# Kernel tuning notes

Hardware: AMD Instinct MI355X
Metric: run time of the kernel (lower is better)

The kernel has to match this reference:

```python
import jax, jax.numpy as jnp
import numpy as np

N = 33554432  # 2**25 activations, 128 MB fp32
K = 1024      # winners kept


def setup_inputs() -> dict:
    key = jax.random.key(0)
    inputs = jax.random.normal(key, (N,), dtype=jnp.float32)
    return {"inputs": inputs, "k": K}


def reference(inputs, k):
    # k-th largest value = threshold (original: tf.sort desc, take element k-1)
    topk_vals, _ = jax.lax.top_k(inputs, k)
    threshold = topk_vals[k - 1]
    # zero out everything strictly below the threshold
    return jnp.where(inputs < threshold, jnp.zeros_like(inputs), inputs)
```

## Files before the change

kernel.cpp:

```cpp
#include <hip/hip_runtime.h>
#include <stdint.h>


#define HIST_BINS 4096
#define CTRL_OFF  HIST_BINS
#define CAND_OFF  (HIST_BINS + 16)

__device__ __forceinline__ uint32_t f2key(float x) {
  uint32_t u = __float_as_uint(x);
  return (u & 0x80000000u) ? ~u : (u | 0x80000000u);
}
__device__ __forceinline__ float key2f(uint32_t k) {
  uint32_t u = (k & 0x80000000u) ? (k & 0x7fffffffu) : ~k;
  return __uint_as_float(u);
}

__global__ void k_hist(const float4* __restrict__ in, int n4, int ntail,
                       const float* __restrict__ in_s,
                       uint32_t* __restrict__ ghist) {
  __shared__ uint32_t lh[HIST_BINS];
  for (int i = threadIdx.x; i < HIST_BINS; i += blockDim.x) lh[i] = 0;
  __syncthreads();
  int stride = gridDim.x * blockDim.x;
  for (int i = blockIdx.x * blockDim.x + threadIdx.x; i < n4; i += stride) {
    float4 v = in[i];
    atomicAdd(&lh[f2key(v.x) >> 20], 1u);
    atomicAdd(&lh[f2key(v.y) >> 20], 1u);
    atomicAdd(&lh[f2key(v.z) >> 20], 1u);
    atomicAdd(&lh[f2key(v.w) >> 20], 1u);
  }
  if (blockIdx.x == 0 && (int)threadIdx.x < ntail)
    atomicAdd(&lh[f2key(in_s[n4 * 4 + threadIdx.x]) >> 20], 1u);
  __syncthreads();
  for (int i = threadIdx.x; i < HIST_BINS; i += blockDim.x) {
    uint32_t c = lh[i];
    if (c) atomicAdd(&ghist[i], c);
  }
}

__global__ void k_select_bucket(const uint32_t* __restrict__ gh,
                                const int* __restrict__ kptr,
                                uint32_t* __restrict__ ctrl) {
  __shared__ uint32_t chunk[256];
  const int CPT = HIST_BINS / 256;
  int t = threadIdx.x;
  uint32_t s = 0;
  for (int i = 0; i < CPT; i++) s += gh[t * CPT + i];
  chunk[t] = s;
  __syncthreads();
  if (t == 0) {
    uint32_t K = (uint32_t)kptr[0];
    uint32_t above = 0;
    int sel = 0;
    for (int c = 255; c >= 0; c--) {
      if (above + chunk[c] >= K) { sel = c; break; }
      above += chunk[c];
    }
    int bsel = sel * CPT;
    for (int b = sel * CPT + CPT - 1; b >= sel * CPT; b--) {
      uint32_t c = gh[b];
      if (above + c >= K) { bsel = b; break; }
      above += c;
    }
    ctrl[1] = (uint32_t)bsel;
    ctrl[2] = K - above;
  }
}

__global__ void k_apply_gather(const float4* __restrict__ in,
                               float4* __restrict__ out, int n4, int ntail,
                               const float* __restrict__ in_s,
                               float* __restrict__ out_s,
                               uint32_t* __restrict__ ctrl,
                               uint32_t* __restrict__ keys,
                               uint32_t* __restrict__ idxs, uint32_t cap) {
  uint32_t sel = ctrl[1];
  int stride = gridDim.x * blockDim.x;
  for (int i = blockIdx.x * blockDim.x + threadIdx.x; i < n4; i += stride) {
    float4 v = in[i];
    uint32_t k0 = f2key(v.x), k1 = f2key(v.y), k2 = f2key(v.z), k3 = f2key(v.w);
    uint32_t b0 = k0 >> 20, b1 = k1 >> 20, b2 = k2 >> 20, b3 = k3 >> 20;
    float4 r;
    r.x = (b0 > sel) ? v.x : 0.0f;
    r.y = (b1 > sel) ? v.y : 0.0f;
    r.z = (b2 > sel) ? v.z : 0.0f;
    r.w = (b3 > sel) ? v.w : 0.0f;
    if (b0 == sel) { uint32_t p = atomicAdd(&ctrl[0], 1u); if (p < cap) { keys[p] = k0; idxs[p] = 4u * i + 0u; } }
    if (b1 == sel) { uint32_t p = atomicAdd(&ctrl[0], 1u); if (p < cap) { keys[p] = k1; idxs[p] = 4u * i + 1u; } }
    if (b2 == sel) { uint32_t p = atomicAdd(&ctrl[0], 1u); if (p < cap) { keys[p] = k2; idxs[p] = 4u * i + 2u; } }
    if (b3 == sel) { uint32_t p = atomicAdd(&ctrl[0], 1u); if (p < cap) { keys[p] = k3; idxs[p] = 4u * i + 3u; } }
    __builtin_nontemporal_store(r.x, &((float*)&out[i])[0]);
    __builtin_nontemporal_store(r.y, &((float*)&out[i])[1]);
    __builtin_nontemporal_store(r.z, &((float*)&out[i])[2]);
    __builtin_nontemporal_store(r.w, &((float*)&out[i])[3]);
  }
  if (blockIdx.x == 0 && (int)threadIdx.x < ntail) {
    int j = n4 * 4 + threadIdx.x;
    float x = in_s[j];
    uint32_t kk = f2key(x);
    uint32_t bb = kk >> 20;
    out_s[j] = (bb > sel) ? x : 0.0f;
    if (bb == sel) { uint32_t p = atomicAdd(&ctrl[0], 1u); if (p < cap) { keys[p] = kk; idxs[p] = (uint32_t)j; } }
  }
}

__global__ void __launch_bounds__(1024) k_final(uint32_t* __restrict__ ctrl,
                                                const uint32_t* __restrict__ keys,
                                                const uint32_t* __restrict__ idxs,
                                                uint32_t cap,
                                                float* __restrict__ out_s) {
  __shared__ uint32_t sh[8192];
  __shared__ uint32_t red[16];
  __shared__ uint32_t s_p, s_want;
  int t = threadIdx.x;
  uint32_t n = ctrl[0]; if (n > cap) n = cap;
  bool useLds = (n <= 8192);
  if (useLds) for (uint32_t i = t; i < n; i += blockDim.x) sh[i] = keys[i];
  if (t == 0) { s_p = ctrl[1] << 20; s_want = ctrl[2]; }
  __syncthreads();
  uint32_t p = s_p, want = s_want;
  for (int bit = 19; bit >= 0; bit--) {
    uint32_t test = p | (1u << bit);
    uint32_t hi = test >> bit;
    uint32_t cnt = 0;
    for (uint32_t i = t; i < n; i += blockDim.x) {
      uint32_t kk = useLds ? sh[i] : keys[i];
      cnt += ((kk >> bit) == hi) ? 1u : 0u;
    }
    for (int off = 32; off; off >>= 1) cnt += __shfl_down((int)cnt, off);
    int wave = t >> 6, lane = t & 63;
    if (lane == 0) red[wave] = cnt;
    __syncthreads();
    if (t == 0) {
      uint32_t tot = 0;
      for (int w = 0; w < 16; w++) tot += red[w];
      if (tot >= want) p = test; else want -= tot;
      s_p = p; s_want = want;
    }
    __syncthreads();
    p = s_p; want = s_want;
  }
  if (t == 0) ctrl[3] = __float_as_uint(key2f(p));
  for (uint32_t i = t; i < n; i += blockDim.x) {
    uint32_t kk = useLds ? sh[i] : keys[i];
    if (kk >= p) out_s[idxs[i]] = key2f(kk);
  }
}

extern "C" void kernel_launch(void* const* d_in, const int* in_sizes, int n_in,
                              void* d_out, int out_size, void* d_ws, size_t ws_size,
                              hipStream_t stream) {
  const float* in = (const float*)d_in[0];
  const int* kptr = (const int*)d_in[1];
  float* out = (float*)d_out;
  int n = in_sizes[0];
  int n4 = n >> 2;
  int ntail = n & 3;

  uint32_t* ws = (uint32_t*)d_ws;
  uint32_t* ghist = ws;
  uint32_t* ctrl = ws + CTRL_OFF;
  size_t ws_words = ws_size / 4;
  uint32_t cap = 0;
  if (ws_words > CAND_OFF + 2) cap = (uint32_t)((ws_words - CAND_OFF) / 2);
  uint32_t* keys = ws + CAND_OFF;
  uint32_t* idxs = keys + cap;

  hipMemsetAsync(d_ws, 0, CAND_OFF * sizeof(uint32_t), stream);

  k_hist<<<1024, 256, 0, stream>>>((const float4*)in, n4, ntail, in, ghist);
  k_select_bucket<<<1, 256, 0, stream>>>(ghist, kptr, ctrl);
  k_apply_gather<<<4096, 256, 0, stream>>>((const float4*)in, (float4*)out,
                                           n4, ntail, in, out, ctrl, keys, idxs, cap);
  k_final<<<1, 1024, 0, stream>>>(ctrl, keys, idxs, cap, out);
}
```

Before: 274.1 us.

## Sample input to bound histogram range, fuse bucket selection via last-block pattern

Adds a sampling kernel that builds a coarse 8-bit histogram from a subset of the input and picks a conservative lower cut bucket. The full 12-bit histogram pass then skips LDS atomics for elements below the cut, removing most of the contention from histogram updates. Bucket selection is folded into the last finishing block of the histogram kernel, which removes a separate launch. A fallback kernel redoes the full histogram if the sample-based cut was too high. The fallback adds an extra launch that exits early, plus a larger memset of the workspace.

```diff
diff --git a/kernel.cpp b/kernel.cpp
--- a/kernel.cpp
+++ b/kernel.cpp
@@ -3,8 +3,21 @@
 
 
 #define HIST_BINS 4096
-#define CTRL_OFF  HIST_BINS
-#define CAND_OFF  (HIST_BINS + 16)
+#define SAMPLE_BLOCKS 64
+#define SAMPLE_F4_PER_BLOCK 1024
+#define SAMPLE_M (SAMPLE_BLOCKS * SAMPLE_F4_PER_BLOCK * 4)
+
+#define TAIL_HIST_OFF 0
+#define FB_HIST_OFF   4096
+#define SAMP_HIST_OFF 8192
+#define DONE_SAMP     8448
+#define DONE_TAIL     8449
+#define DONE_FB       8450
+#define FB_FLAG       8451
+#define B8_OFF        8452
+#define CTRL_OFF      8456
+#define CAND_OFF      8472
+#define ZERO_WORDS    8472
 
 __device__ __forceinline__ uint32_t f2key(float x) {
   uint32_t u = __float_as_uint(x);
@@ -15,55 +28,181 @@
   return __uint_as_float(u);
 }
 
-__global__ void k_hist(const float4* __restrict__ in, int n4, int ntail,
-                       const float* __restrict__ in_s,
-                       uint32_t* __restrict__ ghist) {
+__device__ __forceinline__ void histAdd8(uint32_t* lh, uint32_t bin) {
+  unsigned long long peers = __ballot(1);
+#pragma unroll
+  for (int b = 0; b < 8; b++) {
+    unsigned long long vote = __ballot((bin >> b) & 1u);
+    peers &= ((bin >> b) & 1u) ? vote : ~vote;
+  }
+  unsigned lane = threadIdx.x & 63u;
+  if (lane == (unsigned)(__ffsll((long long)peers) - 1))
+    atomicAdd(&lh[bin], (uint32_t)__popcll(peers));
+}
+
+__device__ void select4096(const uint32_t* __restrict__ gh, uint32_t K,
+                           uint32_t* __restrict__ ctrl,
+                           uint32_t* __restrict__ fbflag,
+                           uint32_t* lh, uint32_t* chunk) {
+  int t = threadIdx.x;
+  for (int i = t; i < HIST_BINS; i += 256) lh[i] = gh[i];
+  __syncthreads();
+  uint32_t s = 0;
+#pragma unroll
+  for (int i = 0; i < 16; i++) s += lh[t * 16 + i];
+  chunk[t] = s;
+  __syncthreads();
+  if (t == 0) {
+    uint32_t above = 0;
+    int sel = -1;
+    for (int c = 255; c >= 0; c--) {
+      if (above + chunk[c] >= K) { sel = c; break; }
+      above += chunk[c];
+    }
+    if (sel < 0) {
+      if (fbflag) { *fbflag = 1u; }
+      else { ctrl[1] = 0u; ctrl[2] = 0xFFFFFFFFu; }
+    } else {
+      int bsel = sel * 16;
+      for (int b = sel * 16 + 15; b >= sel * 16; b--) {
+        uint32_t c = lh[b];
+        if (above + c >= K) { bsel = b; break; }
+        above += c;
+      }
+      ctrl[1] = (uint32_t)bsel;
+      ctrl[2] = K - above;
+    }
+  }
+}
+
+__global__ void k_sample(const float4* __restrict__ in, int n4,
+                         const int* __restrict__ kptr, uint32_t n,
+                         uint32_t* __restrict__ ws) {
+  __shared__ uint32_t lh[256];
+  __shared__ uint32_t s_last;
+  int t = threadIdx.x;
+  if (t < 256) lh[t] = 0;
+  __syncthreads();
+  if (n4 >= SAMPLE_F4_PER_BLOCK) {
+    int chunkf4 = n4 / SAMPLE_BLOCKS;
+    int base = blockIdx.x * chunkf4;
+    if (base + SAMPLE_F4_PER_BLOCK > n4) base = n4 - SAMPLE_F4_PER_BLOCK;
+#pragma unroll
+    for (int j = 0; j < 4; j++) {
+      float4 v = in[base + t + j * 256];
+      histAdd8(lh, f2key(v.x) >> 24);
+      histAdd8(lh, f2key(v.y) >> 24);
+      histAdd8(lh, f2key(v.z) >> 24);
+      histAdd8(lh, f2key(v.w) >> 24);
+    }
+  }
+  __syncthreads();
+  if (t < 256) {
+    uint32_t c = lh[t];
+    if (c) atomicAdd(&ws[SAMP_HIST_OFF + t], c);
+  }
+  __threadfence();
+  if (t == 0) s_last = atomicAdd(&ws[DONE_SAMP], 1u);
+  __syncthreads();
+  if (s_last == SAMPLE_BLOCKS - 1) {
+    __threadfence();
+    if (t < 256) lh[t] = ws[SAMP_HIST_OFF + t];
+    __syncthreads();
+    if (t == 0) {
+      int kv = kptr[0];
+      uint32_t K = (kv < 1) ? 1u : (uint32_t)kv;
+      uint64_t tgt64 = ((uint64_t)K * SAMPLE_M / (n ? n : 1u)) * 2u + 4096u;
+      uint32_t target = (tgt64 > SAMPLE_M) ? (uint32_t)SAMPLE_M : (uint32_t)tgt64;
+      if (target < 4096u) target = 4096u;
+      uint32_t sum = 0; uint32_t b8 = 0;
+      for (int b = 255; b >= 0; b--) {
+        sum += lh[b];
+        if (sum >= target) { b8 = (uint32_t)b; break; }
+      }
+      ws[B8_OFF] = b8;
+    }
+  }
+}
+
+__global__ void k_hist_tail(const float4* __restrict__ in, int n4, int ntail,
+                            const float* __restrict__ in_s,
+                            const int* __restrict__ kptr,
+                            uint32_t* __restrict__ ws, int nblocks, uint32_t n) {
   __shared__ uint32_t lh[HIST_BINS];
-  for (int i = threadIdx.x; i < HIST_BINS; i += blockDim.x) lh[i] = 0;
-  __syncthreads();
+  __shared__ uint32_t chunk[256];
+  __shared__ uint32_t s_last;
+  int t = threadIdx.x;
+  for (int i = t; i < HIST_BINS; i += blockDim.x) lh[i] = 0;
+  __syncthreads();
+  uint32_t cut = ws[B8_OFF] << 4;
   int stride = gridDim.x * blockDim.x;
-  for (int i = blockIdx.x * blockDim.x + threadIdx.x; i < n4; i += stride) {
+  for (int i = blockIdx.x * blockDim.x + t; i < n4; i += stride) {
+    float4 v = in[i];
+    uint32_t k0 = f2key(v.x) >> 20, k1 = f2key(v.y) >> 20;
+    uint32_t k2 = f2key(v.z) >> 20, k3 = f2key(v.w) >> 20;
+    if (k0 >= cut) atomicAdd(&lh[k0], 1u);
+    if (k1 >= cut) atomicAdd(&lh[k1], 1u);
+    if (k2 >= cut) atomicAdd(&lh[k2], 1u);
+    if (k3 >= cut) atomicAdd(&lh[k3], 1u);
+  }
+  if (blockIdx.x == 0 && t < ntail) {
+    uint32_t kk = f2key(in_s[n4 * 4 + t]) >> 20;
+    if (kk >= cut) atomicAdd(&lh[kk], 1u);
+  }
+  __syncthreads();
+  for (int i = t; i < HIST_BINS; i += blockDim.x) {
+    uint32_t c = lh[i];
+    if (c) atomicAdd(&ws[TAIL_HIST_OFF + i], c);
+  }
+  __threadfence();
+  if (t == 0) s_last = atomicAdd(&ws[DONE_TAIL], 1u);
+  __syncthreads();
+  if (s_last == (uint32_t)(nblocks - 1)) {
+    __threadfence();
+    int kv = kptr[0];
+    uint32_t K = (kv < 1) ? 1u : (uint32_t)kv;
+    if (K > n) K = n;
+    select4096(ws + TAIL_HIST_OFF, K, ws + CTRL_OFF, ws + FB_FLAG, lh, chunk);
+  }
+}
+
+__global__ void k_fb(const float4* __restrict__ in, int n4, int ntail,
+                     const float* __restrict__ in_s,
+                     const int* __restrict__ kptr,
+                     uint32_t* __restrict__ ws, int nblocks, uint32_t n) {
+  __shared__ uint32_t lh[HIST_BINS];
+  __shared__ uint32_t chunk[256];
+  __shared__ uint32_t s_flag, s_last;
+  int t = threadIdx.x;
+  if (t == 0) s_flag = ws[FB_FLAG];
+  __syncthreads();
+  if (!s_flag) return;
+  for (int i = t; i < HIST_BINS; i += blockDim.x) lh[i] = 0;
+  __syncthreads();
+  int stride = gridDim.x * blockDim.x;
+  for (int i = blockIdx.x * blockDim.x + t; i < n4; i += stride) {
     float4 v = in[i];
     atomicAdd(&lh[f2key(v.x) >> 20], 1u);
     atomicAdd(&lh[f2key(v.y) >> 20], 1u);
     atomicAdd(&lh[f2key(v.z) >> 20], 1u);
     atomicAdd(&lh[f2key(v.w) >> 20], 1u);
   }
-  if (blockIdx.x == 0 && (int)threadIdx.x < ntail)
-    atomicAdd(&lh[f2key(in_s[n4 * 4 + threadIdx.x]) >> 20], 1u);
-  __syncthreads();
-  for (int i = threadIdx.x; i < HIST_BINS; i += blockDim.x) {
+  if (blockIdx.x == 0 && t < ntail)
+    atomicAdd(&lh[f2key(in_s[n4 * 4 + t]) >> 20], 1u);
+  __syncthreads();
+  for (int i = t; i < HIST_BINS; i += blockDim.x) {
     uint32_t c = lh[i];
-    if (c) atomicAdd(&ghist[i], c);
-  }
-}
-
-__global__ void k_select_bucket(const uint32_t* __restrict__ gh,
-                                const int* __restrict__ kptr,
-                                uint32_t* __restrict__ ctrl) {
-  __shared__ uint32_t chunk[256];
-  const int CPT = HIST_BINS / 256;
-  int t = threadIdx.x;
-  uint32_t s = 0;
-  for (int i = 0; i < CPT; i++) s += gh[t * CPT + i];
-  chunk[t] = s;
-  __syncthreads();
-  if (t == 0) {
-    uint32_t K = (uint32_t)kptr[0];
-    uint32_t above = 0;
-    int sel = 0;
-    for (int c = 255; c >= 0; c--) {
-      if (above + chunk[c] >= K) { sel = c; break; }
-      above += chunk[c];
-    }
-    int bsel = sel * CPT;
-    for (int b = sel * CPT + CPT - 1; b >= sel * CPT; b--) {
-      uint32_t c = gh[b];
-      if (above + c >= K) { bsel = b; break; }
-      above += c;
-    }
-    ctrl[1] = (uint32_t)bsel;
-    ctrl[2] = K - above;
+    if (c) atomicAdd(&ws[FB_HIST_OFF + i], c);
+  }
+  __threadfence();
+  if (t == 0) s_last = atomicAdd(&ws[DONE_FB], 1u);
+  __syncthreads();
+  if (s_last == (uint32_t)(nblocks - 1)) {
+    __threadfence();
+    int kv = kptr[0];
+    uint32_t K = (kv < 1) ? 1u : (uint32_t)kv;
+    if (K > n) K = n;
+    select4096(ws + FB_HIST_OFF, K, ws + CTRL_OFF, nullptr, lh, chunk);
   }
 }
 
@@ -158,7 +297,6 @@
   int ntail = n & 3;
 
   uint32_t* ws = (uint32_t*)d_ws;
-  uint32_t* ghist = ws;
   uint32_t* ctrl = ws + CTRL_OFF;
   size_t ws_words = ws_size / 4;
   uint32_t cap = 0;
@@ -166,10 +304,15 @@
   uint32_t* keys = ws + CAND_OFF;
   uint32_t* idxs = keys + cap;
 
-  hipMemsetAsync(d_ws, 0, CAND_OFF * sizeof(uint32_t), stream);
-
-  k_hist<<<1024, 256, 0, stream>>>((const float4*)in, n4, ntail, in, ghist);
-  k_select_bucket<<<1, 256, 0, stream>>>(ghist, kptr, ctrl);
+  const int HB = 1024;
+
+  hipMemsetAsync(d_ws, 0, ZERO_WORDS * sizeof(uint32_t), stream);
+  k_sample<<<SAMPLE_BLOCKS, 256, 0, stream>>>((const float4*)in, n4, kptr,
+                                              (uint32_t)n, ws);
+  k_hist_tail<<<HB, 256, 0, stream>>>((const float4*)in, n4, ntail, in, kptr,
+                                      ws, HB, (uint32_t)n);
+  k_fb<<<HB, 256, 0, stream>>>((const float4*)in, n4, ntail, in, kptr,
+                               ws, HB, (uint32_t)n);
   k_apply_gather<<<4096, 256, 0, stream>>>((const float4*)in, (float4*)out,
                                            n4, ntail, in, out, ctrl, keys, idxs, cap);
   k_final<<<1, 1024, 0, stream>>>(ctrl, keys, idxs, cap, out);
```

Result: slower. 365.4 us (+33.3%).

## Replace full histogram pass with sampled cutoff in single cooperative kernel

Applied to the files above, without the earlier changes.

Merges the four launches and memset into one cooperative kernel. A small sample (one float4 per thread) is histogrammed to pick a conservative cutoff. A single streaming pass then writes the output and gathers the few candidates above the cutoff into per-wave slots using ballot/popcount instead of global atomics. An exact radix select over those candidates sets the threshold. This removes the full 128 MB histogram read, but needs a fallback path that does the old full histogram and gather when the sample estimate fails, and it adds several grid-wide syncs.

```diff
diff --git a/kernel.cpp b/kernel.cpp
--- a/kernel.cpp
+++ b/kernel.cpp
@@ -1,10 +1,32 @@
 #include <hip/hip_runtime.h>
+#include <hip/hip_cooperative_groups.h>
 #include <stdint.h>
-
-
-#define HIST_BINS 4096
-#define CTRL_OFF  HIST_BINS
-#define CAND_OFF  (HIST_BINS + 16)
+#include <math.h>
+
+namespace cg = cooperative_groups;
+
+
+#define TPB 256
+#define MAXNB 1024
+#define NWAVES_MAX (MAXNB * TPB / 64)
+#define CAPW 64
+
+#define SH_OFF   0
+#define WCNT_OFF 4096
+#define FBH_OFF  8192
+#define CTRL     12288
+#define ZERO_WORDS 12304
+#define REGK_OFF 12304
+#define REGWORDS (NWAVES_MAX * CAPW)
+#define FBPK_OFF (REGK_OFF + 2 * REGWORDS)
+
+#define C_FLAG 0
+#define C_CUT  1
+#define C_THR  2
+#define C_FB2  3
+#define C_SEL  4
+#define C_WANT 5
+#define C_FBN  6
 
 __device__ __forceinline__ uint32_t f2key(float x) {
   uint32_t u = __float_as_uint(x);
@@ -15,135 +37,337 @@
   return __uint_as_float(u);
 }
 
-__global__ void k_hist(const float4* __restrict__ in, int n4, int ntail,
-                       const float* __restrict__ in_s,
-                       uint32_t* __restrict__ ghist) {
-  __shared__ uint32_t lh[HIST_BINS];
-  for (int i = threadIdx.x; i < HIST_BINS; i += blockDim.x) lh[i] = 0;
+__device__ __forceinline__ void apply1(float4 v, int i, uint32_t cutK,
+                                       float* outp, uint32_t* keysR,
+                                       uint32_t* idxR, uint32_t rbase,
+                                       uint32_t& wcount, uint64_t lt) {
+  uint32_t k0 = f2key(v.x), k1 = f2key(v.y), k2 = f2key(v.z), k3 = f2key(v.w);
+  bool q0 = k0 >= cutK, q1 = k1 >= cutK, q2 = k2 >= cutK, q3 = k3 >= cutK;
+  float* o = outp + 4 * (size_t)i;
+  __builtin_nontemporal_store(q0 ? v.x : 0.0f, o);
+  __builtin_nontemporal_store(q1 ? v.y : 0.0f, o + 1);
+  __builtin_nontemporal_store(q2 ? v.z : 0.0f, o + 2);
+  __builtin_nontemporal_store(q3 ? v.w : 0.0f, o + 3);
+  if (__ballot(q0 | q1 | q2 | q3)) {
+    uint32_t base = 4u * (uint32_t)i;
+    uint64_t m0 = __ballot(q0);
+    if (q0) { uint32_t p = wcount + (uint32_t)__popcll(m0 & lt); if (p < CAPW) { keysR[rbase + p] = k0; idxR[rbase + p] = base; } }
+    wcount += (uint32_t)__popcll(m0);
+    uint64_t m1 = __ballot(q1);
+    if (q1) { uint32_t p = wcount + (uint32_t)__popcll(m1 & lt); if (p < CAPW) { keysR[rbase + p] = k1; idxR[rbase + p] = base + 1u; } }
+    wcount += (uint32_t)__popcll(m1);
+    uint64_t m2 = __ballot(q2);
+    if (q2) { uint32_t p = wcount + (uint32_t)__popcll(m2 & lt); if (p < CAPW) { keysR[rbase + p] = k2; idxR[rbase + p] = base + 2u; } }
+    wcount += (uint32_t)__popcll(m2);
+    uint64_t m3 = __ballot(q3);
+    if (q3) { uint32_t p = wcount + (uint32_t)__popcll(m3 & lt); if (p < CAPW) { keysR[rbase + p] = k3; idxR[rbase + p] = base + 3u; } }
+    wcount += (uint32_t)__popcll(m3);
+  }
+}
+
+__global__ void __launch_bounds__(TPB, 4)
+k_kwta(const float4* __restrict__ in4, float4* __restrict__ out4,
+       int n4, int ntail, const float* __restrict__ in_s,
+       float* __restrict__ out_s, const int* __restrict__ kptr, uint32_t n,
+       uint32_t* __restrict__ ws, uint32_t* __restrict__ keysR,
+       uint32_t* __restrict__ idxR, uint32_t* __restrict__ keysF,
+       uint32_t* __restrict__ idxF, uint32_t fbcap) {
+  cg::grid_group grid = cg::this_grid();
+  __shared__ uint32_t shb[8192];
+  __shared__ uint32_t chunk[256];
+  __shared__ uint32_t pre[256];
+  __shared__ uint32_t red[4];
+  __shared__ uint32_t s_a, s_b;
+  const int t = threadIdx.x;
+  const int b = blockIdx.x;
+  const int nb = gridDim.x;
+  const int T = nb * TPB;
+  const int gtid = b * TPB + t;
+  const int lane = t & 63;
+  const uint64_t lt = (1ULL << lane) - 1ULL;
+
+  for (int i = gtid; i < ZERO_WORDS; i += T) ws[i] = 0u;
+  grid.sync();
+
+  for (int i = t; i < 4096; i += TPB) shb[i] = 0u;
   __syncthreads();
-  int stride = gridDim.x * blockDim.x;
-  for (int i = blockIdx.x * blockDim.x + threadIdx.x; i < n4; i += stride) {
-    float4 v = in[i];
-    atomicAdd(&lh[f2key(v.x) >> 20], 1u);
-    atomicAdd(&lh[f2key(v.y) >> 20], 1u);
-    atomicAdd(&lh[f2key(v.z) >> 20], 1u);
-    atomicAdd(&lh[f2key(v.w) >> 20], 1u);
-  }
-  if (blockIdx.x == 0 && (int)threadIdx.x < ntail)
-    atomicAdd(&lh[f2key(in_s[n4 * 4 + threadIdx.x]) >> 20], 1u);
+  if (n4 >= T) {
+    float4 v = in4[b * (n4 / nb) + t];
+    atomicAdd(&shb[f2key(v.x) >> 20], 1u);
+    atomicAdd(&shb[f2key(v.y) >> 20], 1u);
+    atomicAdd(&shb[f2key(v.z) >> 20], 1u);
+    atomicAdd(&shb[f2key(v.w) >> 20], 1u);
+  }
   __syncthreads();
-  for (int i = threadIdx.x; i < HIST_BINS; i += blockDim.x) {
-    uint32_t c = lh[i];
-    if (c) atomicAdd(&ghist[i], c);
-  }
-}
-
-__global__ void k_select_bucket(const uint32_t* __restrict__ gh,
-                                const int* __restrict__ kptr,
-                                uint32_t* __restrict__ ctrl) {
-  __shared__ uint32_t chunk[256];
-  const int CPT = HIST_BINS / 256;
-  int t = threadIdx.x;
-  uint32_t s = 0;
-  for (int i = 0; i < CPT; i++) s += gh[t * CPT + i];
-  chunk[t] = s;
+  for (int i = t; i < 4096; i += TPB) {
+    uint32_t c = shb[i];
+    if (c) atomicAdd(&ws[SH_OFF + i], c);
+  }
+  grid.sync();
+
+  if (b == 0) {
+    for (int i = t; i < 4096; i += TPB) shb[i] = ws[SH_OFF + i];
+    __syncthreads();
+    uint32_t s = 0;
+#pragma unroll
+    for (int i = 0; i < 16; i++) s += shb[t * 16 + i];
+    chunk[t] = s;
+    __syncthreads();
+    if (t == 0) {
+      int kv = kptr[0];
+      uint32_t K = kv < 1 ? 1u : (uint32_t)kv;
+      if (K > n) K = n;
+      double M = (double)T * 4.0;
+      double A = (double)K * M / (double)(n ? n : 1u);
+      double x = 4.0 + sqrt(A + 24.0);
+      uint32_t smin = (uint32_t)(x * x) + 1u;
+      if (smin < 64u) smin = 64u;
+      uint32_t acc = 0, cut = 0;
+      for (int c = 255; c >= 0; c--) {
+        if (acc + chunk[c] >= smin) {
+          for (int b2 = c * 16 + 15; b2 >= c * 16; b2--) {
+            acc += shb[b2];
+            if (acc >= smin) { cut = (uint32_t)b2; break; }
+          }
+          break;
+        }
+        acc += chunk[c];
+      }
+      ws[CTRL + C_CUT] = cut;
+    }
+  }
+  grid.sync();
+
+  {
+    const uint32_t cutK = ws[CTRL + C_CUT] << 20;
+    const int wave = gtid >> 6;
+    const uint32_t rbase = (uint32_t)wave * CAPW;
+    uint32_t wcount = 0;
+    int i = gtid;
+    for (; i + 3 * T < n4; i += 4 * T) {
+      float4 v0 = in4[i];
+      float4 v1 = in4[i + T];
+      float4 v2 = in4[i + 2 * T];
+      float4 v3 = in4[i + 3 * T];
+      apply1(v0, i, cutK, (float*)out4, keysR, idxR, rbase, wcount, lt);
+      apply1(v1, i + T, cutK, (float*)out4, keysR, idxR, rbase, wcount, lt);
+      apply1(v2, i + 2 * T, cutK, (float*)out4, keysR, idxR, rbase, wcount, lt);
+      apply1(v3, i + 3 * T, cutK, (float*)out4, keysR, idxR, rbase, wcount, lt);
+    }
+    for (; i < n4; i += T) {
+      float4 v = in4[i];
+      apply1(v, i, cutK, (float*)out4, keysR, idxR, rbase, wcount, lt);
+    }
+    if (b == 0 && (t >> 6) == 0) {
+      int j = n4 * 4 + lane;
+      bool q = false;
+      uint32_t kk = 0;
+      if (lane < ntail) {
+        float x = in_s[j];
+        kk = f2key(x);
+        q = kk >= cutK;
+        out_s[j] = q ? x : 0.0f;
+      }
+      uint64_t mq = __ballot(q);
+      if (q) { uint32_t p = wcount + (uint32_t)__popcll(mq & lt); if (p < CAPW) { keysR[rbase + p] = kk; idxR[rbase + p] = (uint32_t)j; } }
+      wcount += (uint32_t)__popcll(mq);
+    }
+    if (lane == 0) {
+      ws[WCNT_OFF + wave] = wcount;
+      if (wcount > CAPW) atomicOr(&ws[CTRL + C_FLAG], 1u);
+    }
+  }
+  grid.sync();
+
+  if (b == 0) {
+    int kv = kptr[0];
+    uint32_t K = kv < 1 ? 1u : (uint32_t)kv;
+    if (K > n) K = n;
+    uint32_t csum = 0;
+    for (int r = t * 16; r < t * 16 + 16; r++) {
+      uint32_t c = ws[WCNT_OFF + r];
+      csum += (c > CAPW ? CAPW : c);
+    }
+    chunk[t] = csum;
+    __syncthreads();
+    if (t == 0) {
+      uint32_t acc = 0;
+      for (int j = 0; j < 256; j++) { uint32_t c = chunk[j]; pre[j] = acc; acc += c; }
+      s_a = acc;
+    }
+    __syncthreads();
+    uint32_t tot = s_a;
+    bool dofb = (ws[CTRL + C_FLAG] != 0u) || (tot < K) || (tot > 8192u);
+    __syncthreads();
+    if (!dofb) {
+      uint32_t off = pre[t];
+      for (int r = t * 16; r < t * 16 + 16; r++) {
+        uint32_t c = ws[WCNT_OFF + r];
+        for (uint32_t j = 0; j < c; j++) shb[off + j] = keysR[(uint32_t)r * CAPW + j];
+        off += c;
+      }
+      __syncthreads();
+      uint32_t p = 0, want = K;
+      for (int bit = 31; bit >= 0; bit--) {
+        uint32_t test = p | (1u << bit), hi = test >> bit, cnt = 0;
+        for (uint32_t ii = t; ii < tot; ii += TPB) cnt += ((shb[ii] >> bit) == hi) ? 1u : 0u;
+        for (int o2 = 32; o2; o2 >>= 1) cnt += __shfl_down((int)cnt, o2);
+        if (lane == 0) red[t >> 6] = cnt;
+        __syncthreads();
+        if (t == 0) {
+          uint32_t tc = red[0] + red[1] + red[2] + red[3];
+          if (tc >= want) p = test; else want -= tc;
+          s_a = p; s_b = want;
+        }
+        __syncthreads();
+        p = s_a; want = s_b;
+      }
+      for (int r = t * 16; r < t * 16 + 16; r++) {
+        uint32_t c = ws[WCNT_OFF + r];
+        for (uint32_t j = 0; j < c; j++) {
+          uint32_t kk = keysR[(uint32_t)r * CAPW + j];
+          if (kk < p) out_s[idxR[(uint32_t)r * CAPW + j]] = 0.0f;
+        }
+      }
+      if (t == 0) ws[CTRL + C_THR] = p;
+    }
+    if (t == 0) ws[CTRL + C_FB2] = dofb ? 1u : 0u;
+  }
+  grid.sync();
+
+  if (ws[CTRL + C_FB2] == 0u) return;
+
+  for (int i = t; i < 4096; i += TPB) shb[i] = 0u;
   __syncthreads();
-  if (t == 0) {
-    uint32_t K = (uint32_t)kptr[0];
-    uint32_t above = 0;
-    int sel = 0;
-    for (int c = 255; c >= 0; c--) {
-      if (above + chunk[c] >= K) { sel = c; break; }
-      above += chunk[c];
-    }
-    int bsel = sel * CPT;
-    for (int b = sel * CPT + CPT - 1; b >= sel * CPT; b--) {
-      uint32_t c = gh[b];
-      if (above + c >= K) { bsel = b; break; }
-      above += c;
-    }
-    ctrl[1] = (uint32_t)bsel;
-    ctrl[2] = K - above;
-  }
-}
-
-__global__ void k_apply_gather(const float4* __restrict__ in,
-                               float4* __restrict__ out, int n4, int ntail,
-                               const float* __restrict__ in_s,
-                               float* __restrict__ out_s,
-                               uint32_t* __restrict__ ctrl,
-                               uint32_t* __restrict__ keys,
-                               uint32_t* __restrict__ idxs, uint32_t cap) {
-  uint32_t sel = ctrl[1];
-  int stride = gridDim.x * blockDim.x;
-  for (int i = blockIdx.x * blockDim.x + threadIdx.x; i < n4; i += stride) {
-    float4 v = in[i];
-    uint32_t k0 = f2key(v.x), k1 = f2key(v.y), k2 = f2key(v.z), k3 = f2key(v.w);
-    uint32_t b0 = k0 >> 20, b1 = k1 >> 20, b2 = k2 >> 20, b3 = k3 >> 20;
-    float4 r;
-    r.x = (b0 > sel) ? v.x : 0.0f;
-    r.y = (b1 > sel) ? v.y : 0.0f;
-    r.z = (b2 > sel) ? v.z : 0.0f;
-    r.w = (b3 > sel) ? v.w : 0.0f;
-    if (b0 == sel) { uint32_t p = atomicAdd(&ctrl[0], 1u); if (p < cap) { keys[p] = k0; idxs[p] = 4u * i + 0u; } }
-    if (b1 == sel) { uint32_t p = atomicAdd(&ctrl[0], 1u); if (p < cap) { keys[p] = k1; idxs[p] = 4u * i + 1u; } }
-    if (b2 == sel) { uint32_t p = atomicAdd(&ctrl[0], 1u); if (p < cap) { keys[p] = k2; idxs[p] = 4u * i + 2u; } }
-    if (b3 == sel) { uint32_t p = atomicAdd(&ctrl[0], 1u); if (p < cap) { keys[p] = k3; idxs[p] = 4u * i + 3u; } }
-    __builtin_nontemporal_store(r.x, &((float*)&out[i])[0]);
-    __builtin_nontemporal_store(r.y, &((float*)&out[i])[1]);
-    __builtin_nontemporal_store(r.z, &((float*)&out[i])[2]);
-    __builtin_nontemporal_store(r.w, &((float*)&out[i])[3]);
-  }
-  if (blockIdx.x == 0 && (int)threadIdx.x < ntail) {
-    int j = n4 * 4 + threadIdx.x;
-    float x = in_s[j];
-    uint32_t kk = f2key(x);
-    uint32_t bb = kk >> 20;
-    out_s[j] = (bb > sel) ? x : 0.0f;
-    if (bb == sel) { uint32_t p = atomicAdd(&ctrl[0], 1u); if (p < cap) { keys[p] = kk; idxs[p] = (uint32_t)j; } }
-  }
-}
-
-__global__ void __launch_bounds__(1024) k_final(uint32_t* __restrict__ ctrl,
-                                                const uint32_t* __restrict__ keys,
-                                                const uint32_t* __restrict__ idxs,
-                                                uint32_t cap,
-                                                float* __restrict__ out_s) {
-  __shared__ uint32_t sh[8192];
-  __shared__ uint32_t red[16];
-  __shared__ uint32_t s_p, s_want;
-  int t = threadIdx.x;
-  uint32_t n = ctrl[0]; if (n > cap) n = cap;
-  bool useLds = (n <= 8192);
-  if (useLds) for (uint32_t i = t; i < n; i += blockDim.x) sh[i] = keys[i];
-  if (t == 0) { s_p = ctrl[1] << 20; s_want = ctrl[2]; }
+  for (int i = gtid; i < n4; i += T) {
+    float4 v = in4[i];
+    atomicAdd(&shb[f2key(v.x) >> 20], 1u);
+    atomicAdd(&shb[f2key(v.y) >> 20], 1u);
+    atomicAdd(&shb[f2key(v.z) >> 20], 1u);
+    atomicAdd(&shb[f2key(v.w) >> 20], 1u);
+  }
+  if (b == 0 && t < ntail) atomicAdd(&shb[f2key(in_s[n4 * 4 + t]) >> 20], 1u);
   __syncthreads();
-  uint32_t p = s_p, want = s_want;
-  for (int bit = 19; bit >= 0; bit--) {
-    uint32_t test = p | (1u << bit);
-    uint32_t hi = test >> bit;
-    uint32_t cnt = 0;
-    for (uint32_t i = t; i < n; i += blockDim.x) {
-      uint32_t kk = useLds ? sh[i] : keys[i];
-      cnt += ((kk >> bit) == hi) ? 1u : 0u;
-    }
-    for (int off = 32; off; off >>= 1) cnt += __shfl_down((int)cnt, off);
-    int wave = t >> 6, lane = t & 63;
-    if (lane == 0) red[wave] = cnt;
+  for (int i = t; i < 4096; i += TPB) {
+    uint32_t c = shb[i];
+    if (c) atomicAdd(&ws[FBH_OFF + i], c);
+  }
+  grid.sync();
+
+  if (b == 0) {
+    for (int i = t; i < 4096; i += TPB) shb[i] = ws[FBH_OFF + i];
+    __syncthreads();
+    uint32_t s = 0;
+#pragma unroll
+    for (int i = 0; i < 16; i++) s += shb[t * 16 + i];
+    chunk[t] = s;
     __syncthreads();
     if (t == 0) {
-      uint32_t tot = 0;
-      for (int w = 0; w < 16; w++) tot += red[w];
-      if (tot >= want) p = test; else want -= tot;
-      s_p = p; s_want = want;
-    }
-    __syncthreads();
-    p = s_p; want = s_want;
-  }
-  if (t == 0) ctrl[3] = __float_as_uint(key2f(p));
-  for (uint32_t i = t; i < n; i += blockDim.x) {
-    uint32_t kk = useLds ? sh[i] : keys[i];
-    if (kk >= p) out_s[idxs[i]] = key2f(kk);
+      int kv = kptr[0];
+      uint32_t K = kv < 1 ? 1u : (uint32_t)kv;
+      if (K > n) K = n;
+      uint32_t above = 0;
+      int sel = 0;
+      for (int c = 255; c >= 0; c--) {
+        if (above + chunk[c] >= K) { sel = c; break; }
+        above += chunk[c];
+      }
+      int bsel = sel * 16;
+      for (int b2 = sel * 16 + 15; b2 >= sel * 16; b2--) {
+        uint32_t c = shb[b2];
+        if (above + c >= K) { bsel = b2; break; }
+        above += c;
+      }
+      ws[CTRL + C_SEL] = (uint32_t)bsel;
+      ws[CTRL + C_WANT] = K - above;
+    }
+  }
+  grid.sync();
+
+  {
+    uint32_t sel = ws[CTRL + C_SEL];
+    for (int i = gtid; i < n4; i += T) {
+      float4 v = in4[i];
+      uint32_t k0 = f2key(v.x), k1 = f2key(v.y), k2 = f2key(v.z), k3 = f2key(v.w);
+      uint32_t b0 = k0 >> 20, b1 = k1 >> 20, b2 = k2 >> 20, b3 = k3 >> 20;
+      float4 r;
+      r.x = (b0 > sel) ? v.x : 0.0f;
+      r.y = (b1 > sel) ? v.y : 0.0f;
+      r.z = (b2 > sel) ? v.z : 0.0f;
+      r.w = (b3 > sel) ? v.w : 0.0f;
+      out4[i] = r;
+      uint32_t base = 4u * (uint32_t)i;
+      if (b0 == sel) { uint32_t p = atomicAdd(&ws[CTRL + C_FBN], 1u); if (p < fbcap) { keysF[p] = k0; idxF[p] = base; } }
+      if (b1 == sel) { uint32_t p = atomicAdd(&ws[CTRL + C_FBN], 1u); if (p < fbcap) { keysF[p] = k1; idxF[p] = base + 1u; } }
+      if (b2 == sel) { uint32_t p = atomicAdd(&ws[CTRL + C_FBN], 1u); if (p < fbcap) { keysF[p] = k2; idxF[p] = base + 2u; } }
+      if (b3 == sel) { uint32_t p = atomicAdd(&ws[CTRL + C_FBN], 1u); if (p < fbcap) { keysF[p] = k3; idxF[p] = base + 3u; } }
+    }
+    if (b == 0 && t < ntail) {
+      int j = n4 * 4 + t;
+      float x = in_s[j];
+      uint32_t kk = f2key(x);
+      uint32_t bb = kk >> 20;
+      out_s[j] = (bb > sel) ? x : 0.0f;
+      if (bb == sel) { uint32_t p = atomicAdd(&ws[CTRL + C_FBN], 1u); if (p < fbcap) { keysF[p] = kk; idxF[p] = (uint32_t)j; } }
+    }
+  }
+  grid.sync();
+
+  if (b == 0) {
+    uint32_t sel = ws[CTRL + C_SEL];
+    uint32_t want = ws[CTRL + C_WANT];
+    uint32_t m = ws[CTRL + C_FBN];
+    bool slow = m > fbcap;
+    uint32_t p = sel << 20;
+    if (!slow) {
+      bool useLds = m <= 8192u;
+      if (useLds) for (uint32_t ii = t; ii < m; ii += TPB) shb[ii] = keysF[ii];
+      __syncthreads();
+      for (int bit = 19; bit >= 0; bit--) {
+        uint32_t test = p | (1u << bit), hi = test >> bit, cnt = 0;
+        for (uint32_t ii = t; ii < m; ii += TPB) {
+          uint32_t kk = useLds ? shb[ii] : keysF[ii];
+          cnt += ((kk >> bit) == hi) ? 1u : 0u;
+        }
+        for (int o2 = 32; o2; o2 >>= 1) cnt += __shfl_down((int)cnt, o2);
+        if (lane == 0) red[t >> 6] = cnt;
+        __syncthreads();
+        if (t == 0) {
+          uint32_t tc = red[0] + red[1] + red[2] + red[3];
+          if (tc >= want) p = test; else want -= tc;
+          s_a = p; s_b = want;
+        }
+        __syncthreads();
+        p = s_a; want = s_b;
+      }
+      for (uint32_t ii = t; ii < m; ii += TPB) {
+        uint32_t kk = useLds ? shb[ii] : keysF[ii];
+        if (kk >= p) out_s[idxF[ii]] = key2f(kk);
+      }
+    } else {
+      for (int bit = 19; bit >= 0; bit--) {
+        uint32_t test = p | (1u << bit), hi = test >> bit, cnt = 0;
+        for (uint32_t ii = t; ii < n; ii += TPB) {
+          uint32_t kk = f2key(in_s[ii]);
+          if ((kk >> 20) == sel) cnt += ((kk >> bit) == hi) ? 1u : 0u;
+        }
+        for (int o2 = 32; o2; o2 >>= 1) cnt += __shfl_down((int)cnt, o2);
+        if (lane == 0) red[t >> 6] = cnt;
+        __syncthreads();
+        if (t == 0) {
+          uint32_t tc = red[0] + red[1] + red[2] + red[3];
+          if (tc >= want) p = test; else want -= tc;
+          s_a = p; s_b = want;
+        }
+        __syncthreads();
+        p = s_a; want = s_b;
+      }
+      for (uint32_t ii = t; ii < n; ii += TPB) {
+        uint32_t kk = f2key(in_s[ii]);
+        if ((kk >> 20) == sel && kk >= p) out_s[ii] = in_s[ii];
+      }
+    }
+    if (t == 0) ws[CTRL + C_THR] = p;
   }
 }
 
@@ -158,19 +382,27 @@
   int ntail = n & 3;
 
   uint32_t* ws = (uint32_t*)d_ws;
-  uint32_t* ghist = ws;
-  uint32_t* ctrl = ws + CTRL_OFF;
-  size_t ws_words = ws_size / 4;
-  uint32_t cap = 0;
-  if (ws_words > CAND_OFF + 2) cap = (uint32_t)((ws_words - CAND_OFF) / 2);
-  uint32_t* keys = ws + CAND_OFF;
-  uint32_t* idxs = keys + cap;
-
-  hipMemsetAsync(d_ws, 0, CAND_OFF * sizeof(uint32_t), stream);
-
-  k_hist<<<1024, 256, 0, stream>>>((const float4*)in, n4, ntail, in, ghist);
-  k_select_bucket<<<1, 256, 0, stream>>>(ghist, kptr, ctrl);
-  k_apply_gather<<<4096, 256, 0, stream>>>((const float4*)in, (float4*)out,
-                                           n4, ntail, in, out, ctrl, keys, idxs, cap);
-  k_final<<<1, 1024, 0, stream>>>(ctrl, keys, idxs, cap, out);
+  int64_t ws_words = (int64_t)(ws_size / 4);
+  uint32_t* keysR = ws + REGK_OFF;
+  uint32_t* idxR = keysR + REGWORDS;
+  int64_t rem = ws_words - (int64_t)FBPK_OFF;
+  uint32_t fbcap = rem > 1 ? (uint32_t)(rem / 2) : 0u;
+  uint32_t* keysF = ws + FBPK_OFF;
+  uint32_t* idxF = keysF + fbcap;
+
+  int mb = 0;
+  hipOccupancyMaxActiveBlocksPerMultiprocessor(&mb, k_kwta, TPB, 0);
+  if (mb < 1) mb = 1;
+  int grid = mb * 256;
+  if (grid > MAXNB) grid = MAXNB;
+
+  const float4* in4 = (const float4*)in;
+  float4* out4 = (float4*)out;
+  uint32_t n_u = (uint32_t)n;
+  void* args[] = {(void*)&in4, (void*)&out4, (void*)&n4, (void*)&ntail,
+                  (void*)&in, (void*)&out, (void*)&kptr, (void*)&n_u,
+                  (void*)&ws, (void*)&keysR, (void*)&idxR,
+                  (void*)&keysF, (void*)&idxF, (void*)&fbcap};
+  hipLaunchCooperativeKernel((void*)k_kwta, dim3(grid), dim3(TPB), args, 0,
+                             stream);
 }
```

New measurement: 924.6 us. +237.3%, slower.
